# Optimization experiments

Hardware: AMD Instinct MI355X
Metric: run time of the kernel (lower is better)

## Reference

```python
import jax, jax.numpy as jnp
import numpy as np

VOCAB, HID, L, HEADS, INTER, MAXSEQ, NCLS = 30522, 128, 2, 2, 512, 512, 2
HEAD = HID // HEADS
B, S = 128, 512


def _tlin(x, W, b):
    # TernaryLinear: threshold-quantize W to {-1,0,1} with per-tensor scale,
    # then ordinary linear. delta = 0.7*mean|W|, alpha = mean|W| over kept entries.
    absW = jnp.abs(W)
    delta = 0.7 * jnp.mean(absW)
    mask = (absW > delta).astype(W.dtype)
    alpha = jnp.sum(absW * mask) / jnp.maximum(jnp.sum(mask), 1.0)
    Wq = jnp.sign(W) * mask * alpha  # [out, in]
    return jnp.einsum('...i,oi->...o', x, Wq) + b


def _ln(x, g, b, eps=1e-5):
    m = jnp.mean(x, axis=-1, keepdims=True)
    v = jnp.var(x, axis=-1, keepdims=True)
    return (x - m) * jax.lax.rsqrt(v + eps) * g + b


def setup_inputs() -> dict:
    key = jax.random.key(0)
    ks = iter(jax.random.split(key, 64))
    n = lambda shape, s=0.02: jax.random.normal(next(ks), shape, dtype=jnp.float32) * s
    inp = {
        'input_ids': jax.random.randint(next(ks), (B, S), 0, VOCAB, dtype=jnp.int32).astype(jnp.int64),
        'tok_emb': n((VOCAB, HID)),
        'pos_emb': n((MAXSEQ, HID)),
        'ln_g': jnp.ones((HID,), jnp.float32), 'ln_b': jnp.zeros((HID,), jnp.float32),
        'qw': n((L, HID, HID)), 'qb': jnp.zeros((L, HID), jnp.float32),
        'kw': n((L, HID, HID)), 'kb': jnp.zeros((L, HID), jnp.float32),
        'vw': n((L, HID, HID)), 'vb': jnp.zeros((L, HID), jnp.float32),
        'aow': n((L, HID, HID)), 'aob': jnp.zeros((L, HID), jnp.float32),
        'iw': n((L, INTER, HID)), 'ib': jnp.zeros((L, INTER), jnp.float32),
        'fow': n((L, HID, INTER)), 'fob': jnp.zeros((L, HID), jnp.float32),
        'ln1g': jnp.ones((L, HID), jnp.float32), 'ln1b': jnp.zeros((L, HID), jnp.float32),
        'ln2g': jnp.ones((L, HID), jnp.float32), 'ln2b': jnp.zeros((L, HID), jnp.float32),
        'clf_w': n((NCLS, HID)), 'clf_b': jnp.zeros((NCLS,), jnp.float32),
    }
    return inp


def reference(input_ids, tok_emb, pos_emb, ln_g, ln_b, qw, qb, kw, kb, vw, vb,
              aow, aob, iw, ib, fow, fob, ln1g, ln1b, ln2g, ln2b, clf_w, clf_b):
    b, s = input_ids.shape
    x = tok_emb[input_ids] + pos_emb[jnp.arange(s)][None, :, :]  # [B,S,H]
    x = _ln(x, ln_g, ln_b)
    scale = 1.0 / (HEAD ** 0.5)
    for l in range(L):
        q = _tlin(x, qw[l], qb[l]).reshape(b, s, HEADS, HEAD)
        k = _tlin(x, kw[l], kb[l]).reshape(b, s, HEADS, HEAD)
        v = _tlin(x, vw[l], vb[l]).reshape(b, s, HEADS, HEAD)
        scores = jnp.einsum('bqhd,bkhd->bhqk', q, k) * scale
        attn = jax.nn.softmax(scores, axis=-1)
        ctx = jnp.einsum('bhqk,bkhd->bqhd', attn, v).reshape(b, s, HID)
        attn_out = _tlin(ctx, aow[l], aob[l])
        x = _ln(x + attn_out, ln1g[l], ln1b[l])
        ff = _tlin(jax.nn.relu(_tlin(x, iw[l], ib[l])), fow[l], fob[l])
        x = _ln(x + ff, ln2g[l], ln2b[l])
    cls = x[:, 0, :]
    logits = _tlin(cls, clf_w, clf_b)  # [B, NCLS]
    return logits
```

## Files before the change

kernel.cpp:

```cpp
#include <hip/hip_runtime.h>

typedef short bf8s __attribute__((ext_vector_type(8)));
typedef float f32x4 __attribute__((ext_vector_type(4)));

#define MFMA16(a, b, c) __builtin_amdgcn_mfma_f32_16x16x32_bf16(a, b, c, 0, 0, 0)

constexpr int S_ = 512, HID_ = 128, B_ = 128, M_ = B_ * S_;

__device__ inline short f2bf(float f) {
  unsigned u = __float_as_uint(f);
  u = (u + 0x7fffu + ((u >> 16) & 1u)) >> 16;
  return (short)u;
}
__device__ inline float bf2f(short s) {
  return __uint_as_float(((unsigned)(unsigned short)s) << 16);
}

__device__ __forceinline__ void async16(void* lds, const void* g) {
  __builtin_amdgcn_global_load_lds(
      (const __attribute__((address_space(1))) unsigned int*)g,
      (__attribute__((address_space(3))) unsigned int*)lds, 16, 0, 0);
}

__device__ __forceinline__ bf8s ldsb(const short* base, int byteoff) {
  return *(const bf8s*)((const char*)base + byteoff);
}

__device__ inline float block_red1024(float v, float* red) {
  #pragma unroll
  for (int m = 32; m >= 1; m >>= 1) v += __shfl_xor(v, m);
  __syncthreads();
  if ((threadIdx.x & 63) == 0) red[threadIdx.x >> 6] = v;
  __syncthreads();
  float t = 0.f;
  #pragma unroll
  for (int i = 0; i < 16; ++i) t += red[i];
  return t;
}

__device__ inline void mat_info(int mat, const float* qw, const float* kw,
                                const float* vw, const float* aow, const float* iw,
                                const float* fw, const float* cw,
                                const float** src, int* n, int* doff) {
  if (mat < 6) {
    int l = mat / 3, which = mat % 3;
    const float* t[3] = {qw, kw, vw};
    *src = t[which] + l * 16384; *n = 16384; *doff = l * 49152 + which * 16384;
  } else if (mat < 8) {
    int l = mat - 6;
    *src = aow + l * 16384; *n = 16384; *doff = 98304 + l * 16384;
  } else if (mat < 10) {
    *src = iw + (mat - 8) * 65536; *n = 65536; *doff = 131072 + (mat - 8) * 65536;
  } else if (mat < 12) {
    *src = fw + (mat - 10) * 65536; *n = 65536; *doff = 262144 + (mat - 10) * 65536;
  } else {
    *src = cw; *n = 256; *doff = 393216;
  }
}

__global__ __launch_bounds__(1024) void k_qe(const float* qw, const float* kw,
    const float* vw, const float* aow, const float* iw, const float* fw,
    const float* cw, short* WQ,
    const int* __restrict__ ids, const float* __restrict__ tok,
    const float* __restrict__ pos, const float* __restrict__ g,
    const float* __restrict__ bb, short* xb) {
  __shared__ float red[16];
  int tid = threadIdx.x;
  if (blockIdx.x < 13) {
    const float* src; int n, doff;
    mat_info(blockIdx.x, qw, kw, vw, aow, iw, fw, cw, &src, &n, &doff);
    float s = 0.f;
    for (int i = tid; i < n; i += 1024) s += fabsf(src[i]);
    s = block_red1024(s, red);
    float delta = 0.7f * s / (float)n;
    float s2 = 0.f, c2 = 0.f;
    for (int i = tid; i < n; i += 1024) {
      float a = fabsf(src[i]);
      if (a > delta) { s2 += a; c2 += 1.f; }
    }
    s2 = block_red1024(s2, red);
    c2 = block_red1024(c2, red);
    float alpha = s2 / fmaxf(c2, 1.f);
    for (int i = tid; i < n; i += 1024) {
      float w = src[i];
      WQ[doff + i] = (fabsf(w) > delta) ? f2bf(w > 0.f ? alpha : -alpha) : (short)0;
    }
  } else {
    int wave = tid >> 6, lane = tid & 63;
    int t = (blockIdx.x - 13) * 16 + wave;
    int s = t & (S_ - 1);
    int id = ids[t];
    float e0 = tok[(size_t)id * HID_ + lane] + pos[(size_t)s * HID_ + lane];
    float e1 = tok[(size_t)id * HID_ + 64 + lane] + pos[(size_t)s * HID_ + 64 + lane];
    float sum = e0 + e1, ssq = e0 * e0 + e1 * e1;
    #pragma unroll
    for (int m = 32; m >= 1; m >>= 1) {
      sum += __shfl_xor(sum, m);
      ssq += __shfl_xor(ssq, m);
    }
    float mean = sum / 128.f;
    float var = ssq / 128.f - mean * mean;
    float rs = rsqrtf(var + 1e-5f);
    size_t o = (size_t)t * HID_;
    xb[o + lane]      = f2bf((e0 - mean) * rs * g[lane] + bb[lane]);
    xb[o + 64 + lane] = f2bf((e1 - mean) * rs * g[64 + lane] + bb[64 + lane]);
  }
}

__global__ __launch_bounds__(256) void k_qkv(
    const short* __restrict__ A, const short* __restrict__ W,
    const float* __restrict__ b0, const float* __restrict__ b1,
    const float* __restrict__ b2, short* outb) {
  __shared__ short Wl[128 * 144];
  int tid = threadIdx.x, lane = tid & 63, wave = tid >> 6;
  int row16 = lane & 15, quad = lane >> 4;
  int tok0 = blockIdx.x * 64 + wave * 16;
  int nbase = blockIdx.y * 128;

  const short* arow = A + (size_t)(tok0 + row16) * 128 + quad * 8;
  bf8s av[4];
  #pragma unroll
  for (int ki = 0; ki < 4; ++ki) av[ki] = *(const bf8s*)(arow + ki * 32);

  {
    int r = tid >> 1, half = tid & 1;
    const short* src = W + (size_t)(nbase + r) * 128 + half * 64;
    short* dst = &Wl[r * 144 + half * 64];
    #pragma unroll
    for (int j = 0; j < 8; ++j)
      *(bf8s*)(dst + j * 8) = *(const bf8s*)(src + j * 8);
  }
  __syncthreads();

  f32x4 acc[8] = {};
  #pragma unroll
  for (int ki = 0; ki < 4; ++ki)
    #pragma unroll
    for (int ot = 0; ot < 8; ++ot) {
      bf8s b = *(const bf8s*)(&Wl[(ot * 16 + row16) * 144 + ki * 32 + quad * 8]);
      acc[ot] = MFMA16(av[ki], b, acc[ot]);
    }

  const float* bp = (blockIdx.y == 0) ? b0 : ((blockIdx.y == 1) ? b1 : b2);
  float osc = (blockIdx.y == 0) ? 0.125f : 1.0f;
  int m0 = tok0 + quad * 4;
  #pragma unroll
  for (int ot = 0; ot < 8; ++ot) {
    int col = ot * 16 + row16;
    float bi = bp[col];
    #pragma unroll
    for (int r = 0; r < 4; ++r) {
      float v = (acc[ot][r] + bi) * osc;
      outb[(size_t)(m0 + r) * 384 + nbase + col] = f2bf(v);
    }
  }
}

template <int DOQKV>
__global__ __launch_bounds__(512, 4) void k_aoff(
    const short* __restrict__ cb, const short* __restrict__ Wa,
    const float* __restrict__ aob, const float* __restrict__ ln1g,
    const float* __restrict__ ln1b, const short* __restrict__ Wi,
    const short* __restrict__ Wf, const float* __restrict__ ib,
    const float* __restrict__ fb, const float* __restrict__ ln2g,
    const float* __restrict__ ln2b, short* xb,
    const short* __restrict__ Wqkv2, const float* __restrict__ qb2,
    const float* __restrict__ kb2, const float* __restrict__ vb2,
    short* qkvout) {
  __shared__ short SM[39936];
  int tid = threadIdx.x, lane = tid & 63, wave = tid >> 6;
  int row16 = lane & 15, quad = lane >> 4;
  int tok0 = blockIdx.x * 128 + wave * 16;
  short* mySt = SM + 16384 + wave * 640;
  short* myX  = SM + 21504 + wave * 2304;
  int xr = lane >> 2, xs = (lane & 3) * 32;

  {
    #pragma unroll
    for (int t = 0; t < 4; ++t) {
      int o = (wave * 4 + t) * 1024 + lane * 16;
      int row = o >> 8, off = o & 255;
      async16((char*)SM + (wave * 4 + t) * 1024,
              (const char*)Wa + row * 256 + (off ^ ((row & 7) << 4)));
    }
    const short* src = xb + (size_t)(tok0 + xr) * HID_ + xs;
    bf8s x0 = *(const bf8s*)(src);
    bf8s x1 = *(const bf8s*)(src + 8);
    bf8s x2 = *(const bf8s*)(src + 16);
    bf8s x3 = *(const bf8s*)(src + 24);
    short* dst = myX + xr * 144 + xs;
    *(bf8s*)(dst) = x0;      *(bf8s*)(dst + 8) = x1;
    *(bf8s*)(dst + 16) = x2; *(bf8s*)(dst + 24) = x3;
  }

  const short* arow = cb + (size_t)(tok0 + row16) * 128 + quad * 8;
  bf8s av[4];
  #pragma unroll
  for (int ki = 0; ki < 4; ++ki) av[ki] = *(const bf8s*)(arow + ki * 32);
  __syncthreads();

  f32x4 acc[8] = {};
  #pragma unroll
  for (int ki = 0; ki < 4; ++ki)
    #pragma unroll
    for (int ot = 0; ot < 8; ++ot) {
      int rr = ot * 16 + row16;
      bf8s b = ldsb(SM, rr * 256 + ((ki * 64 + quad * 16) ^ ((rr & 7) << 4)));
      acc[ot] = MFMA16(av[ki], b, acc[ot]);
    }
  __syncthreads();

  {
    int o = wave * 1024 + lane * 16;
    int rw = o >> 8, ow = o & 255;
    async16((char*)SM + wave * 1024,
            (const char*)Wi + (0 * 32 + rw) * 256 + (ow ^ ((rw & 7) << 4)));
    int rf = o >> 6, of = o & 63;
    async16((char*)SM + 16384 + wave * 1024,
            (const char*)Wf + rf * 1024 + 0 * 64 + (of ^ ((rf & 3) << 4)));
  }

  {
    float sum[4] = {}, ssq[4] = {};
    #pragma unroll
    for (int ot = 0; ot < 8; ++ot) {
      int col = ot * 16 + row16;
      float bi = aob[col];
      #pragma unroll
      for (int r = 0; r < 4; ++r) {
        float v = acc[ot][r] + bi + bf2f(myX[(quad * 4 + r) * 144 + col]);
        acc[ot][r] = v;
        sum[r] += v; ssq[r] += v * v;
      }
    }
    #pragma unroll
    for (int m = 1; m <= 8; m <<= 1)
      #pragma unroll
      for (int r = 0; r < 4; ++r) {
        sum[r] += __shfl_xor(sum[r], m);
        ssq[r] += __shfl_xor(ssq[r], m);
      }
    float mean[4], rstd[4];
    #pragma unroll
    for (int r = 0; r < 4; ++r) {
      mean[r] = sum[r] / 128.f;
      float var = ssq[r] / 128.f - mean[r] * mean[r];
      rstd[r] = rsqrtf(var + 1e-5f);
    }
    #pragma unroll
    for (int ot = 0; ot < 8; ++ot) {
      int col = ot * 16 + row16;
      float gg = ln1g[col], bb2 = ln1b[col];
      #pragma unroll
      for (int r = 0; r < 4; ++r)
        acc[ot][r] = (acc[ot][r] - mean[r]) * rstd[r] * gg + bb2;
    }
  }

  #pragma unroll
  for (int ot = 0; ot < 8; ++ot) {
    int col = ot * 16 + row16;
    #pragma unroll
    for (int r = 0; r < 4; ++r)
      myX[(quad * 4 + r) * 144 + col] = f2bf(acc[ot][r]);
  }
  #pragma unroll
  for (int ki = 0; ki < 4; ++ki)
    av[ki] = *(const bf8s*)(myX + row16 * 144 + ki * 32 + quad * 8);
  __syncthreads();

  f32x4 acc2[8] = {};
  for (int c = 0; c < 16; ++c) {
    if (c < 15) {
      int o = wave * 1024 + lane * 16;
      int rw = o >> 8, ow = o & 255;
      async16((char*)SM + ((c + 1) & 1) * 8192 + wave * 1024,
              (const char*)Wi + ((c + 1) * 32 + rw) * 256 + (ow ^ ((rw & 7) << 4)));
      int rf = o >> 6, of = o & 63;
      async16((char*)SM + 16384 + ((c + 1) & 1) * 8192 + wave * 1024,
              (const char*)Wf + rf * 1024 + (c + 1) * 64 + (of ^ ((rf & 3) << 4)));
    } else if (DOQKV) {
      int o = wave * 1024 + lane * 16;
      int rh = o >> 8, ow = o & 255;
      async16((char*)SM + wave * 1024,
              (const char*)Wqkv2 + rh * 256 + (ow ^ ((rh & 7) << 4)));
      int rc = 32 + rh;
      async16((char*)SM + 16384 + wave * 1024,
              (const char*)Wqkv2 + rc * 256 + (ow ^ ((rc & 7) << 4)));
    }

    #pragma unroll
    for (int ot = 0; ot < 2; ++ot) {
      f32x4 hacc = {};
      #pragma unroll
      for (int ki = 0; ki < 4; ++ki) {
        int rr = ot * 16 + row16;
        bf8s b = ldsb(SM, (c & 1) * 8192 + rr * 256 +
                              ((ki * 64 + quad * 16) ^ ((rr & 7) << 4)));
        hacc = MFMA16(av[ki], b, hacc);
      }
      float bi = ib[c * 32 + ot * 16 + row16];
      #pragma unroll
      for (int r = 0; r < 4; ++r)
        mySt[(quad * 4 + r) * 40 + ot * 16 + row16] =
            f2bf(fmaxf(hacc[r] + bi, 0.f));
    }
    bf8s ha = *(const bf8s*)(mySt + row16 * 40 + quad * 8);
    #pragma unroll
    for (int ot = 0; ot < 8; ++ot) {
      int rr = ot * 16 + row16;
      bf8s bB = ldsb(SM, 16384 + (c & 1) * 8192 + rr * 64 +
                             ((quad * 16) ^ ((rr & 3) << 4)));
      acc2[ot] = MFMA16(ha, bB, acc2[ot]);
    }
    __syncthreads();
  }

  {
    float sum[4] = {}, ssq[4] = {};
    #pragma unroll
    for (int ot = 0; ot < 8; ++ot) {
      int col = ot * 16 + row16;
      float bi = fb[col];
      #pragma unroll
      for (int r = 0; r < 4; ++r) {
        float v = acc2[ot][r] + bi + bf2f(myX[(quad * 4 + r) * 144 + col]);
        acc2[ot][r] = v;
        sum[r] += v; ssq[r] += v * v;
      }
    }
    #pragma unroll
    for (int m = 1; m <= 8; m <<= 1)
      #pragma unroll
      for (int r = 0; r < 4; ++r) {
        sum[r] += __shfl_xor(sum[r], m);
        ssq[r] += __shfl_xor(ssq[r], m);
      }
    float mean[4], rstd[4];
    #pragma unroll
    for (int r = 0; r < 4; ++r) {
      mean[r] = sum[r] / 128.f;
      float var = ssq[r] / 128.f - mean[r] * mean[r];
      rstd[r] = rsqrtf(var + 1e-5f);
    }
    #pragma unroll
    for (int ot = 0; ot < 8; ++ot) {
      int col = ot * 16 + row16;
      float gg = ln2g[col], bb2 = ln2b[col];
      #pragma unroll
      for (int r = 0; r < 4; ++r)
        acc2[ot][r] = (acc2[ot][r] - mean[r]) * rstd[r] * gg + bb2;
    }
  }

  #pragma unroll
  for (int ot = 0; ot < 8; ++ot) {
    int col = ot * 16 + row16;
    #pragma unroll
    for (int r = 0; r < 4; ++r)
      myX[(quad * 4 + r) * 144 + col] = f2bf(acc2[ot][r]);
  }
  {
    const short* src = myX + xr * 144 + xs;
    short* dst = xb + (size_t)(tok0 + xr) * HID_ + xs;
    #pragma unroll
    for (int j = 0; j < 4; ++j)
      *(bf8s*)(dst + j * 8) = *(const bf8s*)(src + j * 8);
  }

  if (DOQKV) {
    bf8s av2[4];
    #pragma unroll
    for (int ki = 0; ki < 4; ++ki)
      av2[ki] = *(const bf8s*)(myX + row16 * 144 + ki * 32 + quad * 8);
    for (int j = 0; j < 6; ++j) {
      if (j < 5) {
        int jn = j + 1;
        int o = wave * 1024 + lane * 16;
        int rh = o >> 8, ow = o & 255;
        async16((char*)SM + (jn & 1) * 8192 + wave * 1024,
                (const char*)Wqkv2 + (jn * 64 + rh) * 256 + (ow ^ ((rh & 7) << 4)));
        int rc = 32 + rh;
        async16((char*)SM + 16384 + (jn & 1) * 8192 + wave * 1024,
                (const char*)Wqkv2 + (jn * 64 + rc) * 256 + (ow ^ ((rc & 7) << 4)));
      }
      f32x4 acc3[4] = {};
      #pragma unroll
      for (int ki = 0; ki < 4; ++ki)
        #pragma unroll
        for (int ot = 0; ot < 4; ++ot) {
          int rr = ot * 16 + row16;
          int bb_ = (ot < 2) ? (j & 1) * 8192 : 16384 + (j & 1) * 8192;
          bf8s b = ldsb(SM, bb_ + (rr & 31) * 256 +
                                ((ki * 64 + quad * 16) ^ ((rr & 7) << 4)));
          acc3[ot] = MFMA16(av2[ki], b, acc3[ot]);
        }
      const float* bp = (j < 2) ? qb2 : ((j < 4) ? kb2 : vb2);
      float osc = (j < 2) ? 0.125f : 1.0f;
      #pragma unroll
      for (int ot = 0; ot < 4; ++ot) {
        int col = ot * 16 + row16;
        float bi = bp[(j & 1) * 64 + col];
        #pragma unroll
        for (int r = 0; r < 4; ++r)
          myX[(quad * 4 + r) * 144 + col] = f2bf((acc3[ot][r] + bi) * osc);
      }
      {
        int xr2 = lane >> 2, xs2 = (lane & 3) * 16;
        const short* src = myX + xr2 * 144 + xs2;
        short* dst = qkvout + (size_t)(tok0 + xr2) * 384 + j * 64 + xs2;
        *(bf8s*)(dst) = *(const bf8s*)(src);
        *(bf8s*)(dst + 8) = *(const bf8s*)(src + 8);
      }
      __syncthreads();
    }
  }
}

__global__ __launch_bounds__(512) void k_attn(const short* __restrict__ qkv,
                                              short* __restrict__ O) {
  __shared__ short Kl[64 * 72];
  __shared__ short Vtl[64 * 72];
  __shared__ short Pl[8][16 * 72];

  int tid = threadIdx.x, lane = tid & 63, wave = tid >> 6;
  int row16 = lane & 15, quad = lane >> 4;
  int b = blockIdx.x >> 2, h = (blockIdx.x >> 1) & 1, qhalf = blockIdx.x & 1;
  const short* base  = qkv + (size_t)b * S_ * 384;
  const short* kbase = base + 128 + h * 64;
  const short* vbase = base + 256 + h * 64;
  int q0 = qhalf * 256 + wave * 32;

  bf8s qa[2][2];
  #pragma unroll
  for (int qf = 0; qf < 2; ++qf) {
    const short* qrow = base + h * 64 +
        (size_t)(q0 + qf * 16 + row16) * 384 + quad * 8;
    qa[qf][0] = *(const bf8s*)(qrow);
    qa[qf][1] = *(const bf8s*)(qrow + 32);
  }

  int krow = tid >> 3, dgk = tid & 7;
  int vkey = tid & 63, dgv = tid >> 6;
  const short* kptr = kbase + (size_t)krow * 384 + dgk * 8;
  const short* vptr = vbase + (size_t)vkey * 384 + dgv * 8;
  bf8s kst = *(const bf8s*)(kptr);
  bf8s vst = *(const bf8s*)(vptr);

  float li[2][4] = {};
  f32x4 oacc[2][4] = {};
  short* myP = &Pl[wave][0];

  for (int kt0 = 0; kt0 < S_; kt0 += 64) {
    if (kt0) __syncthreads();
    *(bf8s*)(&Kl[krow * 72 + dgk * 8]) = kst;
    #pragma unroll
    for (int j = 0; j < 8; ++j) Vtl[(dgv * 8 + j) * 72 + vkey] = vst[j];
    __syncthreads();
    if (kt0 + 64 < S_) {
      kst = *(const bf8s*)(kptr + (size_t)(kt0 + 64) * 384);
      vst = *(const bf8s*)(vptr + (size_t)(kt0 + 64) * 384);
    }

    f32x4 sc[2][4] = {};
    #pragma unroll
    for (int ks = 0; ks < 4; ++ks) {
      const short* kp = &Kl[(ks * 16 + row16) * 72 + quad * 8];
      bf8s k0 = *(const bf8s*)(kp);
      bf8s k1 = *(const bf8s*)(kp + 32);
      sc[0][ks] = MFMA16(qa[0][0], k0, sc[0][ks]);
      sc[0][ks] = MFMA16(qa[0][1], k1, sc[0][ks]);
      sc[1][ks] = MFMA16(qa[1][0], k0, sc[1][ks]);
      sc[1][ks] = MFMA16(qa[1][1], k1, sc[1][ks]);
    }

    #pragma unroll
    for (int qf = 0; qf < 2; ++qf) {
      #pragma unroll
      for (int ks = 0; ks < 4; ++ks)
        #pragma unroll
        for (int r = 0; r < 4; ++r) {
          float pv = __expf(sc[qf][ks][r]);
          li[qf][r] += pv;
          myP[(quad * 4 + r) * 72 + ks * 16 + row16] = f2bf(pv);
        }
      bf8s pa0 = *(const bf8s*)(&myP[row16 * 72 + quad * 8]);
      bf8s pa1 = *(const bf8s*)(&myP[row16 * 72 + 32 + quad * 8]);
      #pragma unroll
      for (int dt = 0; dt < 4; ++dt) {
        const short* vp = &Vtl[(dt * 16 + row16) * 72 + quad * 8];
        bf8s v0 = *(const bf8s*)(vp);
        bf8s v1 = *(const bf8s*)(vp + 32);
        oacc[qf][dt] = MFMA16(pa0, v0, oacc[qf][dt]);
        oacc[qf][dt] = MFMA16(pa1, v1, oacc[qf][dt]);
      }
    }
  }

  #pragma unroll
  for (int qf = 0; qf < 2; ++qf) {
    float inv[4];
    #pragma unroll
    for (int r = 0; r < 4; ++r) {
      float t = li[qf][r];
      #pragma unroll
      for (int m = 1; m <= 8; m <<= 1) t += __shfl_xor(t, m);
      inv[r] = 1.f / t;
    }
    size_t trow = (size_t)(b * S_ + q0 + qf * 16 + quad * 4);
    #pragma unroll
    for (int dt = 0; dt < 4; ++dt)
      #pragma unroll
      for (int r = 0; r < 4; ++r)
        O[(trow + r) * HID_ + h * 64 + dt * 16 + row16] =
            f2bf(oacc[qf][dt][r] * inv[r]);
  }
}

__global__ __launch_bounds__(256) void k_clf(const short* __restrict__ xb,
    const short* __restrict__ Wc, const float* __restrict__ cbias, float* out) {
  int i = threadIdx.x;
  int b = i >> 1, c = i & 1;
  float s = 0.f;
  for (int k = 0; k < HID_; ++k)
    s += bf2f(xb[(size_t)b * S_ * HID_ + k]) * bf2f(Wc[c * HID_ + k]);
  out[b * 2 + c] = s + cbias[c];
}

extern "C" void kernel_launch(void* const* d_in, const int* in_sizes, int n_in,
                              void* d_out, int out_size, void* d_ws, size_t ws_size,
                              hipStream_t stream) {
  const int*   ids     = (const int*)d_in[0];
  const float* tok_emb = (const float*)d_in[1];
  const float* pos_emb = (const float*)d_in[2];
  const float* ln_g    = (const float*)d_in[3];
  const float* ln_bb   = (const float*)d_in[4];
  const float* qw      = (const float*)d_in[5];
  const float* qbias   = (const float*)d_in[6];
  const float* kw      = (const float*)d_in[7];
  const float* kbias   = (const float*)d_in[8];
  const float* vw      = (const float*)d_in[9];
  const float* vbias   = (const float*)d_in[10];
  const float* aow     = (const float*)d_in[11];
  const float* aobias  = (const float*)d_in[12];
  const float* iw      = (const float*)d_in[13];
  const float* ibias   = (const float*)d_in[14];
  const float* fow     = (const float*)d_in[15];
  const float* fbias   = (const float*)d_in[16];
  const float* ln1g    = (const float*)d_in[17];
  const float* ln1b    = (const float*)d_in[18];
  const float* ln2g    = (const float*)d_in[19];
  const float* ln2b    = (const float*)d_in[20];
  const float* clfw    = (const float*)d_in[21];
  const float* clfb    = (const float*)d_in[22];

  char* ws = (char*)d_ws;
  short* WQ  = (short*)ws;
  short* xb  = (short*)(ws + 1048576);
  short* qkv = (short*)(ws + 1048576 + 16777216);
  short* cb_ = qkv + (size_t)M_ * 384;

  k_qe<<<13 + M_ / 16, 1024, 0, stream>>>(qw, kw, vw, aow, iw, fow, clfw, WQ,
                                          ids, tok_emb, pos_emb, ln_g, ln_bb, xb);

  const short* Wqkv0 = WQ;
  const short* Wqkv1 = WQ + 49152;
  const short* Wa0   = WQ + 98304;
  const short* Wa1   = WQ + 98304 + 16384;
  const short* Wi0   = WQ + 131072;
  const short* Wi1   = WQ + 131072 + 65536;
  const short* Wf0   = WQ + 262144;
  const short* Wf1   = WQ + 262144 + 65536;

  k_qkv<<<dim3(M_ / 64, 3), 256, 0, stream>>>(
      xb, Wqkv0, qbias, kbias, vbias, qkv);
  k_attn<<<512, 512, 0, stream>>>(qkv, cb_);
  k_aoff<1><<<M_ / 128, 512, 0, stream>>>(
      cb_, Wa0, aobias, ln1g, ln1b, Wi0, Wf0, ibias, fbias, ln2g, ln2b, xb,
      Wqkv1, qbias + HID_, kbias + HID_, vbias + HID_, qkv);
  k_attn<<<512, 512, 0, stream>>>(qkv, cb_);
  k_aoff<0><<<M_ / 128, 512, 0, stream>>>(
      cb_, Wa1, aobias + HID_, ln1g + HID_, ln1b + HID_, Wi1, Wf1,
      ibias + 512, fbias + HID_, ln2g + HID_, ln2b + HID_, xb,
      nullptr, nullptr, nullptr, nullptr, nullptr);

  k_clf<<<1, 256, 0, stream>>>(xb, WQ + 393216, clfb, (float*)d_out);
}
```

Measured before the change: 334.2 us.

## Pre-swizzle quantized weights into MFMA fragment order to simplify LDS loads

The quantization kernel now writes ternary weights in a tiled layout that matches the per-lane fragment order of the 16x16x32 MFMA B operand. The QKV, attention-out and FFN kernels can then copy weight tiles to LDS with contiguous async loads and read fragments at lane*16 offsets, with no XOR swizzle address math. It also removes the padded LDS layout and the register-staged copy in the QKV kernel. The catch is a scattered, less coalesced write pattern in the quantization kernel, and every consumer must agree exactly on the new layout.

Measured after the change: 315.3 us. -5.6%, faster.

```diff
diff --git a/kernel.cpp b/kernel.cpp
--- a/kernel.cpp
+++ b/kernel.cpp
@@ -41,20 +41,23 @@
 __device__ inline void mat_info(int mat, const float* qw, const float* kw,
                                 const float* vw, const float* aow, const float* iw,
                                 const float* fw, const float* cw,
-                                const float** src, int* n, int* doff) {
+                                const float** src, int* n, int* doff, int* lc) {
   if (mat < 6) {
     int l = mat / 3, which = mat % 3;
     const float* t[3] = {qw, kw, vw};
     *src = t[which] + l * 16384; *n = 16384; *doff = l * 49152 + which * 16384;
+    *lc = 7;
   } else if (mat < 8) {
     int l = mat - 6;
-    *src = aow + l * 16384; *n = 16384; *doff = 98304 + l * 16384;
+    *src = aow + l * 16384; *n = 16384; *doff = 98304 + l * 16384; *lc = 7;
   } else if (mat < 10) {
     *src = iw + (mat - 8) * 65536; *n = 65536; *doff = 131072 + (mat - 8) * 65536;
+    *lc = 7;
   } else if (mat < 12) {
     *src = fw + (mat - 10) * 65536; *n = 65536; *doff = 262144 + (mat - 10) * 65536;
+    *lc = 9;
   } else {
-    *src = cw; *n = 256; *doff = 393216;
+    *src = cw; *n = 256; *doff = 393216; *lc = 0;
   }
 }
 
@@ -67,8 +70,8 @@
   __shared__ float red[16];
   int tid = threadIdx.x;
   if (blockIdx.x < 13) {
-    const float* src; int n, doff;
-    mat_info(blockIdx.x, qw, kw, vw, aow, iw, fw, cw, &src, &n, &doff);
+    const float* src; int n, doff, lc;
+    mat_info(blockIdx.x, qw, kw, vw, aow, iw, fw, cw, &src, &n, &doff, &lc);
     float s = 0.f;
     for (int i = tid; i < n; i += 1024) s += fabsf(src[i]);
     s = block_red1024(s, red);
@@ -83,7 +86,15 @@
     float alpha = s2 / fmaxf(c2, 1.f);
     for (int i = tid; i < n; i += 1024) {
       float w = src[i];
-      WQ[doff + i] = (fabsf(w) > delta) ? f2bf(w > 0.f ? alpha : -alpha) : (short)0;
+      short qv = (fabsf(w) > delta) ? f2bf(w > 0.f ? alpha : -alpha) : (short)0;
+      if (lc) {
+        int r = i >> lc, c = i & ((1 << lc) - 1);
+        int fi = ((r >> 4) << (lc + 4)) + ((c >> 5) << 9) +
+                 (((c >> 3) & 3) << 7) + ((r & 15) << 3) + (c & 7);
+        WQ[doff + fi] = qv;
+      } else {
+        WQ[doff + i] = qv;
+      }
     }
   } else {
     int wave = tid >> 6, lane = tid & 63;
@@ -111,25 +122,21 @@
     const short* __restrict__ A, const short* __restrict__ W,
     const float* __restrict__ b0, const float* __restrict__ b1,
     const float* __restrict__ b2, short* outb) {
-  __shared__ short Wl[128 * 144];
+  __shared__ short Wl[16384];
   int tid = threadIdx.x, lane = tid & 63, wave = tid >> 6;
   int row16 = lane & 15, quad = lane >> 4;
   int tok0 = blockIdx.x * 64 + wave * 16;
-  int nbase = blockIdx.y * 128;
+
+  const char* Wm = (const char*)W + blockIdx.y * 32768;
+  #pragma unroll
+  for (int t = 0; t < 8; ++t)
+    async16((char*)Wl + t * 4096 + wave * 1024,
+            Wm + t * 4096 + wave * 1024 + lane * 16);
 
   const short* arow = A + (size_t)(tok0 + row16) * 128 + quad * 8;
   bf8s av[4];
   #pragma unroll
   for (int ki = 0; ki < 4; ++ki) av[ki] = *(const bf8s*)(arow + ki * 32);
-
-  {
-    int r = tid >> 1, half = tid & 1;
-    const short* src = W + (size_t)(nbase + r) * 128 + half * 64;
-    short* dst = &Wl[r * 144 + half * 64];
-    #pragma unroll
-    for (int j = 0; j < 8; ++j)
-      *(bf8s*)(dst + j * 8) = *(const bf8s*)(src + j * 8);
-  }
   __syncthreads();
 
   f32x4 acc[8] = {};
@@ -137,7 +144,7 @@
   for (int ki = 0; ki < 4; ++ki)
     #pragma unroll
     for (int ot = 0; ot < 8; ++ot) {
-      bf8s b = *(const bf8s*)(&Wl[(ot * 16 + row16) * 144 + ki * 32 + quad * 8]);
+      bf8s b = ldsb(Wl, ot * 4096 + ki * 1024 + lane * 16);
       acc[ot] = MFMA16(av[ki], b, acc[ot]);
     }
 
@@ -151,7 +158,7 @@
     #pragma unroll
     for (int r = 0; r < 4; ++r) {
       float v = (acc[ot][r] + bi) * osc;
-      outb[(size_t)(m0 + r) * 384 + nbase + col] = f2bf(v);
+      outb[(size_t)(m0 + r) * 384 + blockIdx.y * 128 + col] = f2bf(v);
     }
   }
 }
@@ -174,15 +181,13 @@
   short* mySt = SM + 16384 + wave * 640;
   short* myX  = SM + 21504 + wave * 2304;
   int xr = lane >> 2, xs = (lane & 3) * 32;
+  int lb = lane * 16;
 
   {
     #pragma unroll
-    for (int t = 0; t < 4; ++t) {
-      int o = (wave * 4 + t) * 1024 + lane * 16;
-      int row = o >> 8, off = o & 255;
-      async16((char*)SM + (wave * 4 + t) * 1024,
-              (const char*)Wa + row * 256 + (off ^ ((row & 7) << 4)));
-    }
+    for (int t = 0; t < 4; ++t)
+      async16((char*)SM + t * 8192 + wave * 1024,
+              (const char*)Wa + t * 8192 + wave * 1024 + lb);
     const short* src = xb + (size_t)(tok0 + xr) * HID_ + xs;
     bf8s x0 = *(const bf8s*)(src);
     bf8s x1 = *(const bf8s*)(src + 8);
@@ -204,20 +209,15 @@
   for (int ki = 0; ki < 4; ++ki)
     #pragma unroll
     for (int ot = 0; ot < 8; ++ot) {
-      int rr = ot * 16 + row16;
-      bf8s b = ldsb(SM, rr * 256 + ((ki * 64 + quad * 16) ^ ((rr & 7) << 4)));
+      bf8s b = ldsb(SM, ot * 4096 + ki * 1024 + lb);
       acc[ot] = MFMA16(av[ki], b, acc[ot]);
     }
   __syncthreads();
 
   {
-    int o = wave * 1024 + lane * 16;
-    int rw = o >> 8, ow = o & 255;
-    async16((char*)SM + wave * 1024,
-            (const char*)Wi + (0 * 32 + rw) * 256 + (ow ^ ((rw & 7) << 4)));
-    int rf = o >> 6, of = o & 63;
+    async16((char*)SM + wave * 1024, (const char*)Wi + wave * 1024 + lb);
     async16((char*)SM + 16384 + wave * 1024,
-            (const char*)Wf + rf * 1024 + 0 * 64 + (of ^ ((rf & 3) << 4)));
+            (const char*)Wf + wave * 16384 + lb);
   }
 
   {
@@ -271,22 +271,17 @@
 
   f32x4 acc2[8] = {};
   for (int c = 0; c < 16; ++c) {
+    int side = c & 1;
     if (c < 15) {
-      int o = wave * 1024 + lane * 16;
-      int rw = o >> 8, ow = o & 255;
-      async16((char*)SM + ((c + 1) & 1) * 8192 + wave * 1024,
-              (const char*)Wi + ((c + 1) * 32 + rw) * 256 + (ow ^ ((rw & 7) << 4)));
-      int rf = o >> 6, of = o & 63;
-      async16((char*)SM + 16384 + ((c + 1) & 1) * 8192 + wave * 1024,
-              (const char*)Wf + rf * 1024 + (c + 1) * 64 + (of ^ ((rf & 3) << 4)));
+      int cn = c + 1, sn = cn & 1;
+      async16((char*)SM + sn * 8192 + wave * 1024,
+              (const char*)Wi + cn * 8192 + wave * 1024 + lb);
+      async16((char*)SM + 16384 + sn * 8192 + wave * 1024,
+              (const char*)Wf + wave * 16384 + cn * 1024 + lb);
     } else if (DOQKV) {
-      int o = wave * 1024 + lane * 16;
-      int rh = o >> 8, ow = o & 255;
-      async16((char*)SM + wave * 1024,
-              (const char*)Wqkv2 + rh * 256 + (ow ^ ((rh & 7) << 4)));
-      int rc = 32 + rh;
+      async16((char*)SM + wave * 1024, (const char*)Wqkv2 + wave * 1024 + lb);
       async16((char*)SM + 16384 + wave * 1024,
-              (const char*)Wqkv2 + rc * 256 + (ow ^ ((rc & 7) << 4)));
+              (const char*)Wqkv2 + 8192 + wave * 1024 + lb);
     }
 
     #pragma unroll
@@ -294,9 +289,7 @@
       f32x4 hacc = {};
       #pragma unroll
       for (int ki = 0; ki < 4; ++ki) {
-        int rr = ot * 16 + row16;
-        bf8s b = ldsb(SM, (c & 1) * 8192 + rr * 256 +
-                              ((ki * 64 + quad * 16) ^ ((rr & 7) << 4)));
+        bf8s b = ldsb(SM, side * 8192 + ot * 4096 + ki * 1024 + lb);
         hacc = MFMA16(av[ki], b, hacc);
       }
       float bi = ib[c * 32 + ot * 16 + row16];
@@ -308,9 +301,7 @@
     bf8s ha = *(const bf8s*)(mySt + row16 * 40 + quad * 8);
     #pragma unroll
     for (int ot = 0; ot < 8; ++ot) {
-      int rr = ot * 16 + row16;
-      bf8s bB = ldsb(SM, 16384 + (c & 1) * 8192 + rr * 64 +
-                             ((quad * 16) ^ ((rr & 3) << 4)));
+      bf8s bB = ldsb(SM, 16384 + side * 8192 + ot * 1024 + lb);
       acc2[ot] = MFMA16(ha, bB, acc2[ot]);
     }
     __syncthreads();
@@ -374,25 +365,22 @@
     for (int ki = 0; ki < 4; ++ki)
       av2[ki] = *(const bf8s*)(myX + row16 * 144 + ki * 32 + quad * 8);
     for (int j = 0; j < 6; ++j) {
+      int side = j & 1;
       if (j < 5) {
-        int jn = j + 1;
-        int o = wave * 1024 + lane * 16;
-        int rh = o >> 8, ow = o & 255;
-        async16((char*)SM + (jn & 1) * 8192 + wave * 1024,
-                (const char*)Wqkv2 + (jn * 64 + rh) * 256 + (ow ^ ((rh & 7) << 4)));
-        int rc = 32 + rh;
-        async16((char*)SM + 16384 + (jn & 1) * 8192 + wave * 1024,
-                (const char*)Wqkv2 + (jn * 64 + rc) * 256 + (ow ^ ((rc & 7) << 4)));
+        int jn = j + 1, sn = jn & 1;
+        async16((char*)SM + sn * 8192 + wave * 1024,
+                (const char*)Wqkv2 + jn * 16384 + wave * 1024 + lb);
+        async16((char*)SM + 16384 + sn * 8192 + wave * 1024,
+                (const char*)Wqkv2 + jn * 16384 + 8192 + wave * 1024 + lb);
       }
       f32x4 acc3[4] = {};
       #pragma unroll
       for (int ki = 0; ki < 4; ++ki)
         #pragma unroll
         for (int ot = 0; ot < 4; ++ot) {
-          int rr = ot * 16 + row16;
-          int bb_ = (ot < 2) ? (j & 1) * 8192 : 16384 + (j & 1) * 8192;
-          bf8s b = ldsb(SM, bb_ + (rr & 31) * 256 +
-                                ((ki * 64 + quad * 16) ^ ((rr & 7) << 4)));
+          int bb_ = (ot < 2) ? side * 8192 + ot * 4096
+                             : 16384 + side * 8192 + (ot - 2) * 4096;
+          bf8s b = ldsb(SM, bb_ + ki * 1024 + lb);
           acc3[ot] = MFMA16(av2[ki], b, acc3[ot]);
         }
       const float* bp = (j < 2) ? qb2 : ((j < 4) ? kb2 : vb2);
```
